# Kernel optimization log

Hardware: AMD Instinct MI355X
Metric: run time of the kernel (lower is better)

The kernel has to match this reference:

```python
import jax, jax.numpy as jnp
import numpy as np

N_NODES = 50000
N_EDGES = 800000
D_IN = 96
D_HID = 96
D_OUT = 4


def _glorot(key, shape):
    lim = float(np.sqrt(6.0 / (shape[0] + shape[1])))
    return jax.random.uniform(key, shape, jnp.float32, -lim, lim)


def setup_inputs() -> dict:
    key = jax.random.key(0)
    ks = jax.random.split(key, 8)
    x = jax.random.normal(ks[0], (N_NODES, D_IN), jnp.float32)
    edge_index = jax.random.randint(ks[1], (2, N_EDGES), 0, N_NODES, jnp.int64)
    return {
        'x': x,
        'edge_index': edge_index,
        'W0': _glorot(ks[2], (D_IN, D_HID)), 'b0': jnp.zeros((D_HID,), jnp.float32),
        'W1': _glorot(ks[3], (D_HID, D_HID)), 'b1': jnp.zeros((D_HID,), jnp.float32),
        'W2': _glorot(ks[4], (D_HID, D_HID)), 'b2': jnp.zeros((D_HID,), jnp.float32),
        'Wfc': _glorot(ks[5], (D_HID, D_OUT)), 'bfc': jnp.zeros((D_OUT,), jnp.float32),
    }


def _gcn_conv(x, src, dst, W, b, n):
    # GCNConv: linear transform, add self-loops, symmetric degree norm, scatter-add.
    h = x @ W                                   # [N, D]
    loops = jnp.arange(n, dtype=src.dtype)
    s = jnp.concatenate([src, loops])           # [E+N]
    d = jnp.concatenate([dst, loops])
    deg = jax.ops.segment_sum(jnp.ones_like(d, dtype=h.dtype), d, num_segments=n)
    dinv = jnp.where(deg > 0, jax.lax.rsqrt(deg), 0.0)
    norm = dinv[s] * dinv[d]                    # [E+N]
    msgs = h[s] * norm[:, None]                 # gather + scale
    out = jax.ops.segment_sum(msgs, d, num_segments=n)  # scatter-add
    return out + b


def reference(x, edge_index, W0, b0, W1, b1, W2, b2, Wfc, bfc):
    src, dst = edge_index[0], edge_index[1]
    n = x.shape[0]
    h = jax.nn.relu(_gcn_conv(x, src, dst, W0, b0, n))   # dropout = identity (eval)
    h = jax.nn.relu(_gcn_conv(h, src, dst, W1, b1, n))
    h = jax.nn.relu(_gcn_conv(h, src, dst, W2, b2, n))
    return h @ Wfc + bfc
```

## Files before the change

kernel.cpp:

```cpp
#include <hip/hip_runtime.h>

typedef __bf16 bf16x8 __attribute__((ext_vector_type(8)));
typedef float  f32x4  __attribute__((ext_vector_type(4)));
typedef float  f32x8  __attribute__((ext_vector_type(8)));
typedef unsigned short ushort;
typedef ushort us8 __attribute__((ext_vector_type(8)));

constexpr int N_NODES = 50000;
constexpr int N_EDGES = 800000;
constexpr int SLOTS = 64;
constexpr int GE   = N_EDGES / 256;
constexpr int GMF  = (N_NODES + 63) / 64;
constexpr int ZBLK = (12500 + 255) / 256;
constexpr int WBLK = (3 * 9216) / 256;
constexpr int AGG_NODES = 32;
constexpr int GAGG = (N_NODES + AGG_NODES - 1) / AGG_NODES;

__device__ inline float h16f(ushort u) {
    union { _Float16 h; ushort u; } cv; cv.u = u; return (float)cv.h;
}
__device__ inline ushort f16b(float f) {
    union { _Float16 h; ushort u; } cv; cv.h = (_Float16)f; return cv.u;
}
__device__ inline ushort bf16b(float f) {
    union { __bf16 b; ushort u; } cv; cv.b = (__bf16)f; return cv.u;
}
__device__ inline f32x8 bf8_to_f32(us8 u) {
    f32x8 r;
#pragma unroll
    for (int i = 0; i < 8; ++i) r[i] = __uint_as_float(((unsigned int)u[i]) << 16);
    return r;
}

__global__ __launch_bounds__(256) void k_init(int* __restrict__ cnt,
                                              const float* __restrict__ W0,
                                              const float* __restrict__ W1,
                                              const float* __restrict__ W2,
                                              ushort* __restrict__ Wt) {
    const int b = blockIdx.x;
    const int tid = threadIdx.x;
    if (b < ZBLK) {
        int i = b * 256 + tid;
        if (i < 12500)
            ((uint4*)cnt)[i] = make_uint4(0, 0, 0, 0);
    } else {
        int i = (b - ZBLK) * 256 + tid;
        int m = i / 9216, li = i - m * 9216;
        const float* W = (m == 0) ? W0 : (m == 1) ? W1 : W2;
        int k = li / 96, c = li - k * 96;
        Wt[m * 9216 + c * 96 + k] = bf16b(W[li]);
    }
}

__device__ __forceinline__ void mfma_store(const ushort* sX, const ushort* sW,
                                           ushort* __restrict__ Y, int rowbase) {
    const int tid = threadIdx.x;
    const int wv = tid >> 6, lane = tid & 63, quad = lane >> 4, l16 = lane & 15;
    f32x4 acc[6];
#pragma unroll
    for (int t = 0; t < 6; ++t) acc[t] = (f32x4){0.f, 0.f, 0.f, 0.f};

    const ushort* ax = sX + (wv * 16 + l16) * 96 + quad * 8;
#pragma unroll
    for (int s = 0; s < 3; ++s) {
        bf16x8 a = *(const bf16x8*)(ax + s * 32);
#pragma unroll
        for (int t = 0; t < 6; ++t) {
            bf16x8 b = *(const bf16x8*)(sW + (t * 16 + l16) * 96 + s * 32 + quad * 8);
            acc[t] = __builtin_amdgcn_mfma_f32_16x16x32_bf16(a, b, acc[t], 0, 0, 0);
        }
    }
    const int r0 = rowbase + wv * 16 + quad * 4;
#pragma unroll
    for (int t = 0; t < 6; ++t) {
#pragma unroll
        for (int g = 0; g < 4; ++g) {
            int r = r0 + g;
            if (r < N_NODES) Y[(size_t)r * 96 + t * 16 + l16] = bf16b(acc[t][g]);
        }
    }
}

__global__ __launch_bounds__(256) void k_count_g1(const int* __restrict__ dst,
                                                  int* __restrict__ cnt,
                                                  ushort* __restrict__ rank,
                                                  const float* __restrict__ x,
                                                  const ushort* __restrict__ Wt,
                                                  ushort* __restrict__ H) {
    __shared__ ushort sS[64 * 96 + 96 * 96];
    const int b = blockIdx.x;
    const int tid = threadIdx.x;
    if (b < GMF) {
        ushort* sX = sS;
        ushort* sW = sS + 64 * 96;
        const int rowbase = b * 64;
        for (int i = tid; i < 9216 / 8; i += 256)
            ((uint4*)sW)[i] = ((const uint4*)Wt)[i];
        for (int i = tid; i < 64 * 24; i += 256) {
            int r = i / 24, c4 = i % 24;
            int gr = rowbase + r;
            float4 v = make_float4(0.f, 0.f, 0.f, 0.f);
            if (gr < N_NODES) v = ((const float4*)(x + (size_t)gr * 96))[c4];
            ushort* p = sX + r * 96 + c4 * 4;
            p[0] = bf16b(v.x); p[1] = bf16b(v.y); p[2] = bf16b(v.z); p[3] = bf16b(v.w);
        }
        __syncthreads();
        mfma_store(sX, sW, H, rowbase);
    } else {
        int e = (b - GMF) * 256 + tid;
        rank[e] = (ushort)atomicAdd(&cnt[dst[e]], 1);
    }
}

__global__ __launch_bounds__(256) void k_fill(const int* __restrict__ src,
                                              const int* __restrict__ dst,
                                              const int* __restrict__ cnt,
                                              const ushort* __restrict__ rank,
                                              unsigned int* __restrict__ csr) {
    int e = blockIdx.x * 256 + threadIdx.x;
    int s = src[e], d = dst[e];
    float hs = rsqrtf((float)(cnt[s] + 1));
    unsigned int entry = (unsigned int)(ushort)s | ((unsigned int)f16b(hs) << 16);
    csr[(size_t)d * SLOTS + rank[e]] = entry;
}

__global__ __launch_bounds__(384, 4) void k_agg_gemm(const ushort* __restrict__ A,
                                                     const int* __restrict__ cnt,
                                                     const unsigned int* __restrict__ csr,
                                                     const float* __restrict__ bias,
                                                     const ushort* __restrict__ Wt,
                                                     ushort* __restrict__ Y) {
    __shared__ ushort sS[AGG_NODES * 96 + 96 * 96];
    ushort* sX = sS;
    ushort* sW = sS + AGG_NODES * 96;
    const int tid = threadIdx.x;
    const int rowbase = blockIdx.x * AGG_NODES;

    for (int i = tid; i < 9216 / 8; i += 384)
        ((uint4*)sW)[i] = ((const uint4*)Wt)[i];

    const int g = tid / 12;
    const int c = tid - g * 12;
    const int n = rowbase + g;

    f32x8 acc = (f32x8){0.f, 0.f, 0.f, 0.f, 0.f, 0.f, 0.f, 0.f};
    if (n < N_NODES) {
        const int deg = cnt[n];
        const float dn = rsqrtf((float)(deg + 1));
        us8 a0 = *(const us8*)(A + (size_t)n * 96 + c * 8);

        f32x8 nb = (f32x8){0.f, 0.f, 0.f, 0.f, 0.f, 0.f, 0.f, 0.f};
        const unsigned int* row = csr + (size_t)n * SLOTS;
        int j = 0;
        for (; j + 8 <= deg; j += 8) {
            const uint4 q0 = *(const uint4*)(row + j);
            const uint4 q1 = *(const uint4*)(row + j + 4);
            const us8 u0 = *(const us8*)(A + (size_t)(q0.x & 0xFFFFu) * 96 + c * 8);
            const us8 u1 = *(const us8*)(A + (size_t)(q0.y & 0xFFFFu) * 96 + c * 8);
            const us8 u2 = *(const us8*)(A + (size_t)(q0.z & 0xFFFFu) * 96 + c * 8);
            const us8 u3 = *(const us8*)(A + (size_t)(q0.w & 0xFFFFu) * 96 + c * 8);
            const us8 u4 = *(const us8*)(A + (size_t)(q1.x & 0xFFFFu) * 96 + c * 8);
            const us8 u5 = *(const us8*)(A + (size_t)(q1.y & 0xFFFFu) * 96 + c * 8);
            const us8 u6 = *(const us8*)(A + (size_t)(q1.z & 0xFFFFu) * 96 + c * 8);
            const us8 u7 = *(const us8*)(A + (size_t)(q1.w & 0xFFFFu) * 96 + c * 8);
            nb += bf8_to_f32(u0) * h16f((ushort)(q0.x >> 16));
            nb += bf8_to_f32(u1) * h16f((ushort)(q0.y >> 16));
            nb += bf8_to_f32(u2) * h16f((ushort)(q0.z >> 16));
            nb += bf8_to_f32(u3) * h16f((ushort)(q0.w >> 16));
            nb += bf8_to_f32(u4) * h16f((ushort)(q1.x >> 16));
            nb += bf8_to_f32(u5) * h16f((ushort)(q1.y >> 16));
            nb += bf8_to_f32(u6) * h16f((ushort)(q1.z >> 16));
            nb += bf8_to_f32(u7) * h16f((ushort)(q1.w >> 16));
        }
        for (; j + 4 <= deg; j += 4) {
            const uint4 q = *(const uint4*)(row + j);
            const us8 u0 = *(const us8*)(A + (size_t)(q.x & 0xFFFFu) * 96 + c * 8);
            const us8 u1 = *(const us8*)(A + (size_t)(q.y & 0xFFFFu) * 96 + c * 8);
            const us8 u2 = *(const us8*)(A + (size_t)(q.z & 0xFFFFu) * 96 + c * 8);
            const us8 u3 = *(const us8*)(A + (size_t)(q.w & 0xFFFFu) * 96 + c * 8);
            nb += bf8_to_f32(u0) * h16f((ushort)(q.x >> 16));
            nb += bf8_to_f32(u1) * h16f((ushort)(q.y >> 16));
            nb += bf8_to_f32(u2) * h16f((ushort)(q.z >> 16));
            nb += bf8_to_f32(u3) * h16f((ushort)(q.w >> 16));
        }
        for (; j < deg; ++j) {
            const unsigned int e = row[j];
            const us8 u = *(const us8*)(A + (size_t)(e & 0xFFFFu) * 96 + c * 8);
            nb += bf8_to_f32(u) * h16f((ushort)(e >> 16));
        }
        acc = (nb + bf8_to_f32(a0) * dn) * dn;
#pragma unroll
        for (int f = 0; f < 8; ++f) acc[f] = fmaxf(acc[f] + bias[c * 8 + f], 0.0f);
    }
    {
        us8 o;
#pragma unroll
        for (int f = 0; f < 8; ++f) o[f] = bf16b(acc[f]);
        *(us8*)(sX + g * 96 + c * 8) = o;
    }
    __syncthreads();

    const int wv = tid >> 6;
    const int lane = tid & 63, quad = lane >> 4, l16 = lane & 15;
    const int t0 = 2 * wv;
    const int rg = t0 / 6;
    const int ct0 = t0 - rg * 6;

    f32x4 acc0 = (f32x4){0.f, 0.f, 0.f, 0.f};
    f32x4 acc1 = (f32x4){0.f, 0.f, 0.f, 0.f};
    const ushort* ax = sX + (rg * 16 + l16) * 96 + quad * 8;
#pragma unroll
    for (int s = 0; s < 3; ++s) {
        bf16x8 a = *(const bf16x8*)(ax + s * 32);
        bf16x8 b0 = *(const bf16x8*)(sW + (ct0 * 16 + l16) * 96 + s * 32 + quad * 8);
        bf16x8 b1 = *(const bf16x8*)(sW + ((ct0 + 1) * 16 + l16) * 96 + s * 32 + quad * 8);
        acc0 = __builtin_amdgcn_mfma_f32_16x16x32_bf16(a, b0, acc0, 0, 0, 0);
        acc1 = __builtin_amdgcn_mfma_f32_16x16x32_bf16(a, b1, acc1, 0, 0, 0);
    }
    const int r0 = rowbase + rg * 16 + quad * 4;
#pragma unroll
    for (int gg = 0; gg < 4; ++gg) {
        int r = r0 + gg;
        if (r < N_NODES) {
            Y[(size_t)r * 96 + ct0 * 16 + l16]       = bf16b(acc0[gg]);
            Y[(size_t)r * 96 + (ct0 + 1) * 16 + l16] = bf16b(acc1[gg]);
        }
    }
}

__global__ __launch_bounds__(192) void k_agg_fc(const ushort* __restrict__ A,
                                                const int* __restrict__ cnt,
                                                const unsigned int* __restrict__ csr,
                                                const float* __restrict__ bias,
                                                float* __restrict__ out4,
                                                const float* __restrict__ Wfc,
                                                const float* __restrict__ bfc) {
    __shared__ float sWfc[384];
    __shared__ float red[16][12][4];
    const int tid = threadIdx.x;
    for (int i = tid; i < 384; i += 192) sWfc[i] = Wfc[i];
    __syncthreads();
    const int g = tid / 12, c = tid % 12;
    const int n = blockIdx.x * 16 + g;

    const int deg = cnt[n];
    const float dn = rsqrtf((float)(deg + 1));
    us8 a0 = *(const us8*)(A + (size_t)n * 96 + c * 8);

    f32x8 nb = (f32x8){0.f, 0.f, 0.f, 0.f, 0.f, 0.f, 0.f, 0.f};
    const unsigned int* row = csr + (size_t)n * SLOTS;
    int j = 0;
    for (; j + 8 <= deg; j += 8) {
        const uint4 q0 = *(const uint4*)(row + j);
        const uint4 q1 = *(const uint4*)(row + j + 4);
        const us8 u0 = *(const us8*)(A + (size_t)(q0.x & 0xFFFFu) * 96 + c * 8);
        const us8 u1 = *(const us8*)(A + (size_t)(q0.y & 0xFFFFu) * 96 + c * 8);
        const us8 u2 = *(const us8*)(A + (size_t)(q0.z & 0xFFFFu) * 96 + c * 8);
        const us8 u3 = *(const us8*)(A + (size_t)(q0.w & 0xFFFFu) * 96 + c * 8);
        const us8 u4 = *(const us8*)(A + (size_t)(q1.x & 0xFFFFu) * 96 + c * 8);
        const us8 u5 = *(const us8*)(A + (size_t)(q1.y & 0xFFFFu) * 96 + c * 8);
        const us8 u6 = *(const us8*)(A + (size_t)(q1.z & 0xFFFFu) * 96 + c * 8);
        const us8 u7 = *(const us8*)(A + (size_t)(q1.w & 0xFFFFu) * 96 + c * 8);
        nb += bf8_to_f32(u0) * h16f((ushort)(q0.x >> 16));
        nb += bf8_to_f32(u1) * h16f((ushort)(q0.y >> 16));
        nb += bf8_to_f32(u2) * h16f((ushort)(q0.z >> 16));
        nb += bf8_to_f32(u3) * h16f((ushort)(q0.w >> 16));
        nb += bf8_to_f32(u4) * h16f((ushort)(q1.x >> 16));
        nb += bf8_to_f32(u5) * h16f((ushort)(q1.y >> 16));
        nb += bf8_to_f32(u6) * h16f((ushort)(q1.z >> 16));
        nb += bf8_to_f32(u7) * h16f((ushort)(q1.w >> 16));
    }
    for (; j + 4 <= deg; j += 4) {
        const uint4 q = *(const uint4*)(row + j);
        const us8 u0 = *(const us8*)(A + (size_t)(q.x & 0xFFFFu) * 96 + c * 8);
        const us8 u1 = *(const us8*)(A + (size_t)(q.y & 0xFFFFu) * 96 + c * 8);
        const us8 u2 = *(const us8*)(A + (size_t)(q.z & 0xFFFFu) * 96 + c * 8);
        const us8 u3 = *(const us8*)(A + (size_t)(q.w & 0xFFFFu) * 96 + c * 8);
        nb += bf8_to_f32(u0) * h16f((ushort)(q.x >> 16));
        nb += bf8_to_f32(u1) * h16f((ushort)(q.y >> 16));
        nb += bf8_to_f32(u2) * h16f((ushort)(q.z >> 16));
        nb += bf8_to_f32(u3) * h16f((ushort)(q.w >> 16));
    }
    for (; j < deg; ++j) {
        const unsigned int e = row[j];
        const us8 u = *(const us8*)(A + (size_t)(e & 0xFFFFu) * 96 + c * 8);
        nb += bf8_to_f32(u) * h16f((ushort)(e >> 16));
    }
    f32x8 acc = (nb + bf8_to_f32(a0) * dn) * dn;
#pragma unroll
    for (int f = 0; f < 8; ++f) acc[f] = fmaxf(acc[f] + bias[c * 8 + f], 0.0f);

    float p0 = 0.f, p1 = 0.f, p2 = 0.f, p3 = 0.f;
#pragma unroll
    for (int f = 0; f < 8; ++f) {
        const float* wr = sWfc + (c * 8 + f) * 4;
        p0 += acc[f] * wr[0];
        p1 += acc[f] * wr[1];
        p2 += acc[f] * wr[2];
        p3 += acc[f] * wr[3];
    }
    red[g][c][0] = p0; red[g][c][1] = p1; red[g][c][2] = p2; red[g][c][3] = p3;
    __syncthreads();
    if (tid < 64) {
        const int gg = tid >> 2, jj = tid & 3;
        float s = bfc[jj];
#pragma unroll
        for (int cc = 0; cc < 12; ++cc) s += red[gg][cc][jj];
        out4[(size_t)(blockIdx.x * 16 + gg) * 4 + jj] = s;
    }
}

extern "C" void kernel_launch(void* const* d_in, const int* in_sizes, int n_in,
                              void* d_out, int out_size, void* d_ws, size_t ws_size,
                              hipStream_t stream) {
    const float* x   = (const float*)d_in[0];
    const int*   ei  = (const int*)d_in[1];
    const int*   src = ei;
    const int*   dst = ei + N_EDGES;
    const float* W0  = (const float*)d_in[2];
    const float* b0  = (const float*)d_in[3];
    const float* W1  = (const float*)d_in[4];
    const float* b1  = (const float*)d_in[5];
    const float* W2  = (const float*)d_in[6];
    const float* b2  = (const float*)d_in[7];
    const float* Wfc = (const float*)d_in[8];
    const float* bfc = (const float*)d_in[9];
    float* out = (float*)d_out;

    char* w = (char*)d_ws;
    unsigned int* csr = (unsigned int*)w;  w += ((size_t)N_NODES * SLOTS * 4 + 15) & ~15ULL;
    int*    cnt  = (int*)w;                w += ((size_t)N_NODES * 4 + 15) & ~15ULL;
    ushort* rank = (ushort*)w;             w += ((size_t)N_EDGES * 2 + 15) & ~15ULL;
    ushort* Wt   = (ushort*)w;             w += ((size_t)3 * 9216 * 2 + 15) & ~15ULL;
    ushort* H    = (ushort*)w;             w += ((size_t)N_NODES * 96 * 2 + 15) & ~15ULL;
    ushort* G    = (ushort*)w;

    hipLaunchKernelGGL(k_init, dim3(ZBLK + WBLK), dim3(256), 0, stream,
                       cnt, W0, W1, W2, Wt);
    hipLaunchKernelGGL(k_count_g1, dim3(GMF + GE), dim3(256), 0, stream,
                       dst, cnt, rank, x, Wt, H);
    hipLaunchKernelGGL(k_fill, dim3(GE), dim3(256), 0, stream,
                       src, dst, cnt, rank, csr);
    hipLaunchKernelGGL(k_agg_gemm, dim3(GAGG), dim3(384), 0, stream,
                       H, cnt, csr, b0, Wt + 9216, G);
    hipLaunchKernelGGL(k_agg_gemm, dim3(GAGG), dim3(384), 0, stream,
                       G, cnt, csr, b1, Wt + 2 * 9216, H);
    hipLaunchKernelGGL(k_agg_fc, dim3(N_NODES / 16), dim3(192), 0, stream,
                       H, cnt, csr, b2, out, Wfc, bfc);
}
```

Baseline: 217.7 us.

## Store hidden features in 32-column slabs and aggregate slab-by-slab

Hidden feature matrices now use a slab layout: three planes of N×32 bf16, so each node row is 64 bytes per slab. The aggregation kernels gather one slab at a time across all neighbours, with 4 threads per node, and a barrier between slabs. The aim is to shrink the gathered working set so it stays cache-resident and each gather is a contiguous 64-byte line. In exchange, the CSR row is re-read three times, and the extra barriers plus the lower thread count per node may reduce memory-level parallelism.

```diff
diff --git a/kernel.cpp b/kernel.cpp
--- a/kernel.cpp
+++ b/kernel.cpp
@@ -13,8 +13,9 @@
 constexpr int GMF  = (N_NODES + 63) / 64;
 constexpr int ZBLK = (12500 + 255) / 256;
 constexpr int WBLK = (3 * 9216) / 256;
-constexpr int AGG_NODES = 32;
-constexpr int GAGG = (N_NODES + AGG_NODES - 1) / AGG_NODES;
+constexpr int FCN  = 48;
+constexpr int GFC  = (N_NODES + FCN - 1) / FCN;
+constexpr size_t SLAB = (size_t)N_NODES * 32;
 
 __device__ inline float h16f(ushort u) {
     union { _Float16 h; ushort u; } cv; cv.u = u; return (float)cv.h;
@@ -52,8 +53,8 @@
     }
 }
 
-__device__ __forceinline__ void mfma_store(const ushort* sX, const ushort* sW,
-                                           ushort* __restrict__ Y, int rowbase) {
+__device__ __forceinline__ void mfma_store_slab(const ushort* sX, const ushort* sW,
+                                                ushort* __restrict__ Y, int rowbase) {
     const int tid = threadIdx.x;
     const int wv = tid >> 6, lane = tid & 63, quad = lane >> 4, l16 = lane & 15;
     f32x4 acc[6];
@@ -73,10 +74,11 @@
     const int r0 = rowbase + wv * 16 + quad * 4;
 #pragma unroll
     for (int t = 0; t < 6; ++t) {
+        ushort* base = Y + (size_t)(t >> 1) * SLAB + (t & 1) * 16 + l16;
 #pragma unroll
         for (int g = 0; g < 4; ++g) {
             int r = r0 + g;
-            if (r < N_NODES) Y[(size_t)r * 96 + t * 16 + l16] = bf16b(acc[t][g]);
+            if (r < N_NODES) base[(size_t)r * 32] = bf16b(acc[t][g]);
         }
     }
 }
@@ -105,7 +107,7 @@
             p[0] = bf16b(v.x); p[1] = bf16b(v.y); p[2] = bf16b(v.z); p[3] = bf16b(v.w);
         }
         __syncthreads();
-        mfma_store(sX, sW, H, rowbase);
+        mfma_store_slab(sX, sW, H, rowbase);
     } else {
         int e = (b - GMF) * 256 + tid;
         rank[e] = (ushort)atomicAdd(&cnt[dst[e]], 1);
@@ -124,108 +126,88 @@
     csr[(size_t)d * SLOTS + rank[e]] = entry;
 }
 
-__global__ __launch_bounds__(384, 4) void k_agg_gemm(const ushort* __restrict__ A,
+__global__ __launch_bounds__(256, 4) void k_agg_gemm(const ushort* __restrict__ A,
                                                      const int* __restrict__ cnt,
                                                      const unsigned int* __restrict__ csr,
                                                      const float* __restrict__ bias,
                                                      const ushort* __restrict__ Wt,
                                                      ushort* __restrict__ Y) {
-    __shared__ ushort sS[AGG_NODES * 96 + 96 * 96];
+    __shared__ ushort sS[64 * 96 + 96 * 96];
     ushort* sX = sS;
-    ushort* sW = sS + AGG_NODES * 96;
-    const int tid = threadIdx.x;
-    const int rowbase = blockIdx.x * AGG_NODES;
-
-    for (int i = tid; i < 9216 / 8; i += 384)
+    ushort* sW = sS + 64 * 96;
+    const int tid = threadIdx.x;
+    const int rowbase = blockIdx.x * 64;
+
+    for (int i = tid; i < 9216 / 8; i += 256)
         ((uint4*)sW)[i] = ((const uint4*)Wt)[i];
 
-    const int g = tid / 12;
-    const int c = tid - g * 12;
+    const int g = tid >> 2;
+    const int c4 = tid & 3;
     const int n = rowbase + g;
-
-    f32x8 acc = (f32x8){0.f, 0.f, 0.f, 0.f, 0.f, 0.f, 0.f, 0.f};
-    if (n < N_NODES) {
-        const int deg = cnt[n];
-        const float dn = rsqrtf((float)(deg + 1));
-        us8 a0 = *(const us8*)(A + (size_t)n * 96 + c * 8);
-
-        f32x8 nb = (f32x8){0.f, 0.f, 0.f, 0.f, 0.f, 0.f, 0.f, 0.f};
-        const unsigned int* row = csr + (size_t)n * SLOTS;
-        int j = 0;
-        for (; j + 8 <= deg; j += 8) {
-            const uint4 q0 = *(const uint4*)(row + j);
-            const uint4 q1 = *(const uint4*)(row + j + 4);
-            const us8 u0 = *(const us8*)(A + (size_t)(q0.x & 0xFFFFu) * 96 + c * 8);
-            const us8 u1 = *(const us8*)(A + (size_t)(q0.y & 0xFFFFu) * 96 + c * 8);
-            const us8 u2 = *(const us8*)(A + (size_t)(q0.z & 0xFFFFu) * 96 + c * 8);
-            const us8 u3 = *(const us8*)(A + (size_t)(q0.w & 0xFFFFu) * 96 + c * 8);
-            const us8 u4 = *(const us8*)(A + (size_t)(q1.x & 0xFFFFu) * 96 + c * 8);
-            const us8 u5 = *(const us8*)(A + (size_t)(q1.y & 0xFFFFu) * 96 + c * 8);
-            const us8 u6 = *(const us8*)(A + (size_t)(q1.z & 0xFFFFu) * 96 + c * 8);
-            const us8 u7 = *(const us8*)(A + (size_t)(q1.w & 0xFFFFu) * 96 + c * 8);
-            nb += bf8_to_f32(u0) * h16f((ushort)(q0.x >> 16));
-            nb += bf8_to_f32(u1) * h16f((ushort)(q0.y >> 16));
-            nb += bf8_to_f32(u2) * h16f((ushort)(q0.z >> 16));
-            nb += bf8_to_f32(u3) * h16f((ushort)(q0.w >> 16));
-            nb += bf8_to_f32(u4) * h16f((ushort)(q1.x >> 16));
-            nb += bf8_to_f32(u5) * h16f((ushort)(q1.y >> 16));
-            nb += bf8_to_f32(u6) * h16f((ushort)(q1.z >> 16));
-            nb += bf8_to_f32(u7) * h16f((ushort)(q1.w >> 16));
-        }
-        for (; j + 4 <= deg; j += 4) {
-            const uint4 q = *(const uint4*)(row + j);
-            const us8 u0 = *(const us8*)(A + (size_t)(q.x & 0xFFFFu) * 96 + c * 8);
-            const us8 u1 = *(const us8*)(A + (size_t)(q.y & 0xFFFFu) * 96 + c * 8);
-            const us8 u2 = *(const us8*)(A + (size_t)(q.z & 0xFFFFu) * 96 + c * 8);
-            const us8 u3 = *(const us8*)(A + (size_t)(q.w & 0xFFFFu) * 96 + c * 8);
-            nb += bf8_to_f32(u0) * h16f((ushort)(q.x >> 16));
-            nb += bf8_to_f32(u1) * h16f((ushort)(q.y >> 16));
-            nb += bf8_to_f32(u2) * h16f((ushort)(q.z >> 16));
-            nb += bf8_to_f32(u3) * h16f((ushort)(q.w >> 16));
-        }
-        for (; j < deg; ++j) {
-            const unsigned int e = row[j];
-            const us8 u = *(const us8*)(A + (size_t)(e & 0xFFFFu) * 96 + c * 8);
-            nb += bf8_to_f32(u) * h16f((ushort)(e >> 16));
-        }
-        acc = (nb + bf8_to_f32(a0) * dn) * dn;
-#pragma unroll
-        for (int f = 0; f < 8; ++f) acc[f] = fmaxf(acc[f] + bias[c * 8 + f], 0.0f);
-    }
-    {
-        us8 o;
-#pragma unroll
-        for (int f = 0; f < 8; ++f) o[f] = bf16b(acc[f]);
-        *(us8*)(sX + g * 96 + c * 8) = o;
-    }
-    __syncthreads();
-
-    const int wv = tid >> 6;
-    const int lane = tid & 63, quad = lane >> 4, l16 = lane & 15;
-    const int t0 = 2 * wv;
-    const int rg = t0 / 6;
-    const int ct0 = t0 - rg * 6;
-
-    f32x4 acc0 = (f32x4){0.f, 0.f, 0.f, 0.f};
-    f32x4 acc1 = (f32x4){0.f, 0.f, 0.f, 0.f};
-    const ushort* ax = sX + (rg * 16 + l16) * 96 + quad * 8;
-#pragma unroll
-    for (int s = 0; s < 3; ++s) {
-        bf16x8 a = *(const bf16x8*)(ax + s * 32);
-        bf16x8 b0 = *(const bf16x8*)(sW + (ct0 * 16 + l16) * 96 + s * 32 + quad * 8);
-        bf16x8 b1 = *(const bf16x8*)(sW + ((ct0 + 1) * 16 + l16) * 96 + s * 32 + quad * 8);
-        acc0 = __builtin_amdgcn_mfma_f32_16x16x32_bf16(a, b0, acc0, 0, 0, 0);
-        acc1 = __builtin_amdgcn_mfma_f32_16x16x32_bf16(a, b1, acc1, 0, 0, 0);
-    }
-    const int r0 = rowbase + rg * 16 + quad * 4;
-#pragma unroll
-    for (int gg = 0; gg < 4; ++gg) {
-        int r = r0 + gg;
-        if (r < N_NODES) {
-            Y[(size_t)r * 96 + ct0 * 16 + l16]       = bf16b(acc0[gg]);
-            Y[(size_t)r * 96 + (ct0 + 1) * 16 + l16] = bf16b(acc1[gg]);
-        }
-    }
+    const bool valid = (n < N_NODES);
+
+    int deg = 0; float dn = 1.0f;
+    const unsigned int* row = csr + (size_t)n * SLOTS;
+    if (valid) { deg = cnt[n]; dn = rsqrtf((float)(deg + 1)); }
+
+#pragma unroll
+    for (int p = 0; p < 3; ++p) {
+        const ushort* Ap = A + (size_t)p * SLAB + c4 * 8;
+        f32x8 acc = (f32x8){0.f, 0.f, 0.f, 0.f, 0.f, 0.f, 0.f, 0.f};
+        if (valid) {
+            us8 a0 = *(const us8*)(Ap + (size_t)n * 32);
+            f32x8 nb = (f32x8){0.f, 0.f, 0.f, 0.f, 0.f, 0.f, 0.f, 0.f};
+            int j = 0;
+            for (; j + 8 <= deg; j += 8) {
+                const uint4 q0 = *(const uint4*)(row + j);
+                const uint4 q1 = *(const uint4*)(row + j + 4);
+                const us8 u0 = *(const us8*)(Ap + (size_t)(q0.x & 0xFFFFu) * 32);
+                const us8 u1 = *(const us8*)(Ap + (size_t)(q0.y & 0xFFFFu) * 32);
+                const us8 u2 = *(const us8*)(Ap + (size_t)(q0.z & 0xFFFFu) * 32);
+                const us8 u3 = *(const us8*)(Ap + (size_t)(q0.w & 0xFFFFu) * 32);
+                const us8 u4 = *(const us8*)(Ap + (size_t)(q1.x & 0xFFFFu) * 32);
+                const us8 u5 = *(const us8*)(Ap + (size_t)(q1.y & 0xFFFFu) * 32);
+                const us8 u6 = *(const us8*)(Ap + (size_t)(q1.z & 0xFFFFu) * 32);
+                const us8 u7 = *(const us8*)(Ap + (size_t)(q1.w & 0xFFFFu) * 32);
+                nb += bf8_to_f32(u0) * h16f((ushort)(q0.x >> 16));
+                nb += bf8_to_f32(u1) * h16f((ushort)(q0.y >> 16));
+                nb += bf8_to_f32(u2) * h16f((ushort)(q0.z >> 16));
+                nb += bf8_to_f32(u3) * h16f((ushort)(q0.w >> 16));
+                nb += bf8_to_f32(u4) * h16f((ushort)(q1.x >> 16));
+                nb += bf8_to_f32(u5) * h16f((ushort)(q1.y >> 16));
+                nb += bf8_to_f32(u6) * h16f((ushort)(q1.z >> 16));
+                nb += bf8_to_f32(u7) * h16f((ushort)(q1.w >> 16));
+            }
+            for (; j + 4 <= deg; j += 4) {
+                const uint4 q = *(const uint4*)(row + j);
+                const us8 u0 = *(const us8*)(Ap + (size_t)(q.x & 0xFFFFu) * 32);
+                const us8 u1 = *(const us8*)(Ap + (size_t)(q.y & 0xFFFFu) * 32);
+                const us8 u2 = *(const us8*)(Ap + (size_t)(q.z & 0xFFFFu) * 32);
+                const us8 u3 = *(const us8*)(Ap + (size_t)(q.w & 0xFFFFu) * 32);
+                nb += bf8_to_f32(u0) * h16f((ushort)(q.x >> 16));
+                nb += bf8_to_f32(u1) * h16f((ushort)(q.y >> 16));
+                nb += bf8_to_f32(u2) * h16f((ushort)(q.z >> 16));
+                nb += bf8_to_f32(u3) * h16f((ushort)(q.w >> 16));
+            }
+            for (; j < deg; ++j) {
+                const unsigned int e = row[j];
+                const us8 u = *(const us8*)(Ap + (size_t)(e & 0xFFFFu) * 32);
+                nb += bf8_to_f32(u) * h16f((ushort)(e >> 16));
+            }
+            acc = (nb + bf8_to_f32(a0) * dn) * dn;
+#pragma unroll
+            for (int f = 0; f < 8; ++f) acc[f] = fmaxf(acc[f] + bias[p * 32 + c4 * 8 + f], 0.0f);
+        }
+        {
+            us8 o;
+#pragma unroll
+            for (int f = 0; f < 8; ++f) o[f] = bf16b(acc[f]);
+            *(us8*)(sX + g * 96 + p * 32 + c4 * 8) = o;
+        }
+        __syncthreads();
+    }
+
+    mfma_store_slab(sX, sW, Y, rowbase);
 }
 
 __global__ __launch_bounds__(192) void k_agg_fc(const ushort* __restrict__ A,
@@ -236,77 +218,87 @@
                                                 const float* __restrict__ Wfc,
                                                 const float* __restrict__ bfc) {
     __shared__ float sWfc[384];
-    __shared__ float red[16][12][4];
+    __shared__ float red[FCN][4][4];
     const int tid = threadIdx.x;
     for (int i = tid; i < 384; i += 192) sWfc[i] = Wfc[i];
     __syncthreads();
-    const int g = tid / 12, c = tid % 12;
-    const int n = blockIdx.x * 16 + g;
-
-    const int deg = cnt[n];
-    const float dn = rsqrtf((float)(deg + 1));
-    us8 a0 = *(const us8*)(A + (size_t)n * 96 + c * 8);
-
-    f32x8 nb = (f32x8){0.f, 0.f, 0.f, 0.f, 0.f, 0.f, 0.f, 0.f};
+
+    const int g = tid >> 2, c4 = tid & 3;
+    const int n = blockIdx.x * FCN + g;
+    const bool valid = (n < N_NODES);
+
+    int deg = 0; float dn = 1.0f;
     const unsigned int* row = csr + (size_t)n * SLOTS;
-    int j = 0;
-    for (; j + 8 <= deg; j += 8) {
-        const uint4 q0 = *(const uint4*)(row + j);
-        const uint4 q1 = *(const uint4*)(row + j + 4);
-        const us8 u0 = *(const us8*)(A + (size_t)(q0.x & 0xFFFFu) * 96 + c * 8);
-        const us8 u1 = *(const us8*)(A + (size_t)(q0.y & 0xFFFFu) * 96 + c * 8);
-        const us8 u2 = *(const us8*)(A + (size_t)(q0.z & 0xFFFFu) * 96 + c * 8);
-        const us8 u3 = *(const us8*)(A + (size_t)(q0.w & 0xFFFFu) * 96 + c * 8);
-        const us8 u4 = *(const us8*)(A + (size_t)(q1.x & 0xFFFFu) * 96 + c * 8);
-        const us8 u5 = *(const us8*)(A + (size_t)(q1.y & 0xFFFFu) * 96 + c * 8);
-        const us8 u6 = *(const us8*)(A + (size_t)(q1.z & 0xFFFFu) * 96 + c * 8);
-        const us8 u7 = *(const us8*)(A + (size_t)(q1.w & 0xFFFFu) * 96 + c * 8);
-        nb += bf8_to_f32(u0) * h16f((ushort)(q0.x >> 16));
-        nb += bf8_to_f32(u1) * h16f((ushort)(q0.y >> 16));
-        nb += bf8_to_f32(u2) * h16f((ushort)(q0.z >> 16));
-        nb += bf8_to_f32(u3) * h16f((ushort)(q0.w >> 16));
-        nb += bf8_to_f32(u4) * h16f((ushort)(q1.x >> 16));
-        nb += bf8_to_f32(u5) * h16f((ushort)(q1.y >> 16));
-        nb += bf8_to_f32(u6) * h16f((ushort)(q1.z >> 16));
-        nb += bf8_to_f32(u7) * h16f((ushort)(q1.w >> 16));
-    }
-    for (; j + 4 <= deg; j += 4) {
-        const uint4 q = *(const uint4*)(row + j);
-        const us8 u0 = *(const us8*)(A + (size_t)(q.x & 0xFFFFu) * 96 + c * 8);
-        const us8 u1 = *(const us8*)(A + (size_t)(q.y & 0xFFFFu) * 96 + c * 8);
-        const us8 u2 = *(const us8*)(A + (size_t)(q.z & 0xFFFFu) * 96 + c * 8);
-        const us8 u3 = *(const us8*)(A + (size_t)(q.w & 0xFFFFu) * 96 + c * 8);
-        nb += bf8_to_f32(u0) * h16f((ushort)(q.x >> 16));
-        nb += bf8_to_f32(u1) * h16f((ushort)(q.y >> 16));
-        nb += bf8_to_f32(u2) * h16f((ushort)(q.z >> 16));
-        nb += bf8_to_f32(u3) * h16f((ushort)(q.w >> 16));
-    }
-    for (; j < deg; ++j) {
-        const unsigned int e = row[j];
-        const us8 u = *(const us8*)(A + (size_t)(e & 0xFFFFu) * 96 + c * 8);
-        nb += bf8_to_f32(u) * h16f((ushort)(e >> 16));
-    }
-    f32x8 acc = (nb + bf8_to_f32(a0) * dn) * dn;
-#pragma unroll
-    for (int f = 0; f < 8; ++f) acc[f] = fmaxf(acc[f] + bias[c * 8 + f], 0.0f);
+    if (valid) { deg = cnt[n]; dn = rsqrtf((float)(deg + 1)); }
 
     float p0 = 0.f, p1 = 0.f, p2 = 0.f, p3 = 0.f;
 #pragma unroll
-    for (int f = 0; f < 8; ++f) {
-        const float* wr = sWfc + (c * 8 + f) * 4;
-        p0 += acc[f] * wr[0];
-        p1 += acc[f] * wr[1];
-        p2 += acc[f] * wr[2];
-        p3 += acc[f] * wr[3];
-    }
-    red[g][c][0] = p0; red[g][c][1] = p1; red[g][c][2] = p2; red[g][c][3] = p3;
+    for (int p = 0; p < 3; ++p) {
+        const ushort* Ap = A + (size_t)p * SLAB + c4 * 8;
+        if (valid) {
+            us8 a0 = *(const us8*)(Ap + (size_t)n * 32);
+            f32x8 nb = (f32x8){0.f, 0.f, 0.f, 0.f, 0.f, 0.f, 0.f, 0.f};
+            int j = 0;
+            for (; j + 8 <= deg; j += 8) {
+                const uint4 q0 = *(const uint4*)(row + j);
+                const uint4 q1 = *(const uint4*)(row + j + 4);
+                const us8 u0 = *(const us8*)(Ap + (size_t)(q0.x & 0xFFFFu) * 32);
+                const us8 u1 = *(const us8*)(Ap + (size_t)(q0.y & 0xFFFFu) * 32);
+                const us8 u2 = *(const us8*)(Ap + (size_t)(q0.z & 0xFFFFu) * 32);
+                const us8 u3 = *(const us8*)(Ap + (size_t)(q0.w & 0xFFFFu) * 32);
+                const us8 u4 = *(const us8*)(Ap + (size_t)(q1.x & 0xFFFFu) * 32);
+                const us8 u5 = *(const us8*)(Ap + (size_t)(q1.y & 0xFFFFu) * 32);
+                const us8 u6 = *(const us8*)(Ap + (size_t)(q1.z & 0xFFFFu) * 32);
+                const us8 u7 = *(const us8*)(Ap + (size_t)(q1.w & 0xFFFFu) * 32);
+                nb += bf8_to_f32(u0) * h16f((ushort)(q0.x >> 16));
+                nb += bf8_to_f32(u1) * h16f((ushort)(q0.y >> 16));
+                nb += bf8_to_f32(u2) * h16f((ushort)(q0.z >> 16));
+                nb += bf8_to_f32(u3) * h16f((ushort)(q0.w >> 16));
+                nb += bf8_to_f32(u4) * h16f((ushort)(q1.x >> 16));
+                nb += bf8_to_f32(u5) * h16f((ushort)(q1.y >> 16));
+                nb += bf8_to_f32(u6) * h16f((ushort)(q1.z >> 16));
+                nb += bf8_to_f32(u7) * h16f((ushort)(q1.w >> 16));
+            }
+            for (; j + 4 <= deg; j += 4) {
+                const uint4 q = *(const uint4*)(row + j);
+                const us8 u0 = *(const us8*)(Ap + (size_t)(q.x & 0xFFFFu) * 32);
+                const us8 u1 = *(const us8*)(Ap + (size_t)(q.y & 0xFFFFu) * 32);
+                const us8 u2 = *(const us8*)(Ap + (size_t)(q.z & 0xFFFFu) * 32);
+                const us8 u3 = *(const us8*)(Ap + (size_t)(q.w & 0xFFFFu) * 32);
+                nb += bf8_to_f32(u0) * h16f((ushort)(q.x >> 16));
+                nb += bf8_to_f32(u1) * h16f((ushort)(q.y >> 16));
+                nb += bf8_to_f32(u2) * h16f((ushort)(q.z >> 16));
+                nb += bf8_to_f32(u3) * h16f((ushort)(q.w >> 16));
+            }
+            for (; j < deg; ++j) {
+                const unsigned int e = row[j];
+                const us8 u = *(const us8*)(Ap + (size_t)(e & 0xFFFFu) * 32);
+                nb += bf8_to_f32(u) * h16f((ushort)(e >> 16));
+            }
+            f32x8 acc = (nb + bf8_to_f32(a0) * dn) * dn;
+#pragma unroll
+            for (int f = 0; f < 8; ++f) {
+                float v = fmaxf(acc[f] + bias[p * 32 + c4 * 8 + f], 0.0f);
+                const float* wr = sWfc + (p * 32 + c4 * 8 + f) * 4;
+                p0 += v * wr[0];
+                p1 += v * wr[1];
+                p2 += v * wr[2];
+                p3 += v * wr[3];
+            }
+        }
+        __syncthreads();
+    }
+    red[g][c4][0] = p0; red[g][c4][1] = p1; red[g][c4][2] = p2; red[g][c4][3] = p3;
     __syncthreads();
-    if (tid < 64) {
+    {
         const int gg = tid >> 2, jj = tid & 3;
-        float s = bfc[jj];
-#pragma unroll
-        for (int cc = 0; cc < 12; ++cc) s += red[gg][cc][jj];
-        out4[(size_t)(blockIdx.x * 16 + gg) * 4 + jj] = s;
+        const int nn = blockIdx.x * FCN + gg;
+        if (nn < N_NODES) {
+            float s = bfc[jj];
+#pragma unroll
+            for (int cc = 0; cc < 4; ++cc) s += red[gg][cc][jj];
+            out4[(size_t)nn * 4 + jj] = s;
+        }
     }
 }
 
@@ -341,10 +333,10 @@
                        dst, cnt, rank, x, Wt, H);
     hipLaunchKernelGGL(k_fill, dim3(GE), dim3(256), 0, stream,
                        src, dst, cnt, rank, csr);
-    hipLaunchKernelGGL(k_agg_gemm, dim3(GAGG), dim3(384), 0, stream,
+    hipLaunchKernelGGL(k_agg_gemm, dim3(GMF), dim3(256), 0, stream,
                        H, cnt, csr, b0, Wt + 9216, G);
-    hipLaunchKernelGGL(k_agg_gemm, dim3(GAGG), dim3(384), 0, stream,
+    hipLaunchKernelGGL(k_agg_gemm, dim3(GMF), dim3(256), 0, stream,
                        G, cnt, csr, b1, Wt + 2 * 9216, H);
-    hipLaunchKernelGGL(k_agg_fc, dim3(N_NODES / 16), dim3(192), 0, stream,
+    hipLaunchKernelGGL(k_agg_fc, dim3(GFC), dim3(192), 0, stream,
                        H, cnt, csr, b2, out, Wfc, bfc);
 }
```

After: 224.2 us. 3.0% more time.
